# Performance work log

Hardware: AMD Instinct MI355X
Metric: run time of the kernel (lower is better)

The kernel has to match this reference:

```python
import jax, jax.numpy as jnp
import numpy as np

N_QUBITS = 11
N_CIRCUITS = 3
N_ROTS = 6
BATCH = 512
C64 = jnp.complex64


def _ry_mat(theta):
    # RY(t) = [[cos t/2, -sin t/2], [sin t/2, cos t/2]]
    c = jnp.cos(theta * 0.5)
    s = jnp.sin(theta * 0.5)
    return jnp.stack([jnp.stack([c, -s]), jnp.stack([s, c])]).astype(C64)


def _rz_mat(theta):
    # RZ(t) = diag(e^{-i t/2}, e^{+i t/2})
    e = jnp.exp((-0.5j) * theta.astype(C64))
    z = jnp.zeros_like(e)
    return jnp.stack([jnp.stack([e, z]), jnp.stack([z, jnp.conj(e)])])


def _apply_1q(state, U, q):
    # state: (2,)*n complex; apply 2x2 U on axis q (PennyLane wire q = axis q)
    out = jnp.tensordot(U, state, axes=((1,), (q,)))
    return jnp.moveaxis(out, 0, q)


def _apply_ctrl(state, U, c, t):
    # controlled-U on wires [c(control), t(target)]: block_diag(I2, U) in |c t> basis
    U4 = jnp.eye(4, dtype=C64).at[2:, 2:].set(U)
    out = jnp.tensordot(U4.reshape(2, 2, 2, 2), state, axes=((2, 3), (c, t)))
    return jnp.moveaxis(out, (0, 1), (c, t))


def _simulate(angles):
    # angles: [n_circuits, 6, n_qubits] -> expvals [2*n_qubits] (X then Z)
    n = N_QUBITS
    state = jnp.zeros((2,) * n, dtype=C64).at[(0,) * n].set(1.0)
    for i in range(N_CIRCUITS):
        for q in range(n):
            state = _apply_1q(state, _ry_mat(angles[i, 0, q]), q)
            state = _apply_1q(state, _rz_mat(angles[i, 1, q]), q)
            state = _apply_1q(state, _ry_mat(angles[i, 2, q]), q)
            state = _apply_1q(state, _rz_mat(angles[i, 3, q]), q)
        for q in range(n):
            t = (q + 1) % n
            state = _apply_ctrl(state, _ry_mat(angles[i, 4, q]), q, t)
            state = _apply_ctrl(state, _rz_mat(angles[i, 5, q]), q, t)
    ex_x, ex_z = [], []
    for q in range(n):
        s0 = jnp.take(state, 0, axis=q)
        s1 = jnp.take(state, 1, axis=q)
        # <X_q> = 2 Re <psi_{q=0}|psi_{q=1}>,  <Z_q> = p(q=0) - p(q=1)
        ex_x.append(2.0 * jnp.real(jnp.vdot(s0, s1)))
        ex_z.append(jnp.sum(jnp.abs(s0) ** 2 - jnp.abs(s1) ** 2))
    return jnp.stack(ex_x + ex_z).astype(jnp.float32)


def setup_inputs() -> dict:
    key = jax.random.key(0)
    k1, k2, k3 = jax.random.split(key, 3)
    x = jax.random.normal(k1, (BATCH, N_QUBITS), dtype=jnp.float32)
    W = jax.random.uniform(k2, (N_CIRCUITS, N_QUBITS * N_ROTS, N_QUBITS),
                           dtype=jnp.float32, minval=-0.01, maxval=0.01)
    b = jax.random.uniform(k3, (N_CIRCUITS, N_QUBITS * N_ROTS),
                           dtype=jnp.float32, minval=-0.01, maxval=0.01)
    return {"x": x, "W": W, "b": b}


def reference(x, W, b):
    # per-circuit Linear (dropout is identity in eval): [B, C, n_rots*n_qubits]
    rot = jnp.einsum('coi,bi->bco', W, x) + b[None, :, :]
    angles = rot.reshape(x.shape[0], N_CIRCUITS, N_ROTS, N_QUBITS)
    return jax.vmap(_simulate)(angles)  # [B, 2*n_qubits]
```

## Files before the change

### kernel.cpp

```cpp
#include <hip/hip_runtime.h>

#define NQ 11
#define NC 3
#define NANG (NC * 66)
#define BLOCK 1024

typedef float f2 __attribute__((ext_vector_type(2)));

__device__ __forceinline__ f2 swp(f2 v) { return __builtin_shufflevector(v, v, 1, 0); }

template<int CTRL>
__device__ __forceinline__ float dppx(float v) {
  return __int_as_float(__builtin_amdgcn_update_dpp(
      0, __float_as_int(v), CTRL, 0xF, 0xF, false));
}
template<int CTRL>
__device__ __forceinline__ f2 dpp2(f2 v) {
  f2 r; r.x = dppx<CTRL>(v.x); r.y = dppx<CTRL>(v.y); return r;
}
template<int OFF>
__device__ __forceinline__ float swz1(float v) {
  return __int_as_float(__builtin_amdgcn_ds_swizzle(__float_as_int(v), OFF));
}
template<int OFF>
__device__ __forceinline__ f2 swz2(f2 v) {
  f2 r; r.x = swz1<OFF>(v.x); r.y = swz1<OFF>(v.y); return r;
}
__device__ __forceinline__ float plp16(float v, int lane) {
  auto r = __builtin_amdgcn_permlane16_swap(__float_as_int(v), __float_as_int(v), false, false);
  return __int_as_float((lane & 16) ? r[0] : r[1]);
}
__device__ __forceinline__ float plp32(float v, int lane) {
  auto r = __builtin_amdgcn_permlane32_swap(__float_as_int(v), __float_as_int(v), false, false);
  return __int_as_float((lane & 32) ? r[0] : r[1]);
}
__device__ __forceinline__ f2 plp16_2(f2 v, int lane) {
  f2 r; r.x = plp16(v.x, lane); r.y = plp16(v.y, lane); return r;
}
__device__ __forceinline__ f2 plp32_2(f2 v, int lane) {
  f2 r; r.x = plp32(v.x, lane); r.y = plp32(v.y, lane); return r;
}
__device__ __forceinline__ float plsum16(float v) {
  auto r = __builtin_amdgcn_permlane16_swap(__float_as_int(v), __float_as_int(v), false, false);
  return __int_as_float(r[0]) + __int_as_float(r[1]);
}
__device__ __forceinline__ float plsum32(float v) {
  auto r = __builtin_amdgcn_permlane32_swap(__float_as_int(v), __float_as_int(v), false, false);
  return __int_as_float(r[0]) + __int_as_float(r[1]);
}

__device__ __forceinline__ void apply2p(f2& v0, f2& v1, float4 U) {
  const f2 ai2 = {-U.y, U.y};
  const f2 bi2 = {-U.w, U.w};
  const f2 w0 = swp(v0), w1 = swp(v1);
  const f2 n0 =  U.x * v0 + ai2 * w0 + U.z * v1 + bi2 * w1;
  const f2 n1 = -U.z * v0 + bi2 * w0 + U.x * v1 - ai2 * w1;
  v0 = n0; v1 = n1;
}
__device__ __forceinline__ void gpartp(f2& v, f2 p, float4 U, bool hi) {
  const f2 ai2 = hi ? f2{U.y, -U.y} : f2{-U.y, U.y};
  const float br = hi ? -U.z : U.z;
  const f2 bi2 = {-U.w, U.w};
  v = U.x * v + ai2 * swp(v) + br * p + bi2 * swp(p);
}

template<int WVX>
__device__ __forceinline__ void g_wave(f2& s0, f2& s1, float4 U,
                                       f2* __restrict__ buf, int wave, int lane) {
  const int idx = (wave << 6) | lane;
  buf[idx] = s0; buf[1024 + idx] = s1;
  __syncthreads();
  const int p = ((wave ^ WVX) << 6) | lane;
  const bool hi = (wave & WVX) != 0;
  gpartp(s0, buf[p], U, hi);
  gpartp(s1, buf[1024 + p], U, hi);
}

__global__ __launch_bounds__(BLOCK, 8) void qsim_kernel(
    const float* __restrict__ x, const float* __restrict__ W,
    const float* __restrict__ bias, float* __restrict__ out) {
  const int bidx = blockIdx.x;
  const int tid = threadIdx.x;
  const int lane = tid & 63, wave = tid >> 6;

  __shared__ float xs[NQ];
  __shared__ float ang[NANG];
  __shared__ float4 m1s[NC * NQ];
  __shared__ float4 m2s[NC * NQ];
  __shared__ float4 v1s[NC * 10];
  __shared__ f2 ex0[2048];
  __shared__ f2 ex1[2048];
  __shared__ float red[16][24];

  if (tid < NQ) xs[tid] = x[bidx * NQ + tid];
  __syncthreads();

  if (tid < NANG) {
    const int c = tid / 66, o = tid - c * 66;
    const float* wr = W + (c * 66 + o) * NQ;
    float s = bias[c * 66 + o];
#pragma unroll
    for (int i = 0; i < NQ; ++i) s += wr[i] * xs[i];
    ang[tid] = s;
  }
  __syncthreads();

  if (tid < 2 * NC * NQ) {
    const int kind = tid / (NC * NQ);
    const int id = tid - kind * (NC * NQ);
    const int c = id / NQ, q = id - c * NQ;
    const float* a = ang + c * 66;
    if (kind == 0) {
      float s0,c0,s1,c1,s2,c2,s3,c3;
      sincosf(0.5f*a[q],      &s0,&c0);
      sincosf(0.5f*a[11+q],   &s1,&c1);
      sincosf(0.5f*a[22+q],   &s2,&c2);
      sincosf(0.5f*a[33+q],   &s3,&c3);
      const float mar = c1*c0, mai = -s1*c0;
      const float mbr = -c1*s0, mbi = s1*s0;
      const float nar = c2*mar + s2*mbr, nai = c2*mai - s2*mbi;
      const float nbr = c2*mbr - s2*mar, nbi = c2*mbi + s2*mai;
      m1s[id] = make_float4(c3*nar + s3*nai, c3*nai - s3*nar,
                            c3*nbr + s3*nbi, c3*nbi - s3*nbr);
    } else {
      float s4,c4,s5,c5;
      sincosf(0.5f*a[44+q], &s4,&c4);
      sincosf(0.5f*a[55+q], &s5,&c5);
      m2s[id] = make_float4(c5*c4, -s5*c4, -c5*s4, s5*s4);
    }
  }
  __syncthreads();

  if (tid < NC * 10) {
    const int c = tid / 10, tt = tid - c * 10, t = tt + 1;
    const float4 A = m2s[c*NQ + t - 1];
    const float4 B = m1s[c*NQ + t];
    const float pr_=A.x, pi_=A.y, qr_=A.z, qi_=A.w;
    const float ar_=B.x, ai_=B.y, br_=B.z, bi_=B.w;
    v1s[c*10 + tt] = make_float4(
      (pr_*ar_ - pi_*ai_) - (qr_*br_ + qi_*bi_),
      (pr_*ai_ + pi_*ar_) - (qi_*br_ - qr_*bi_),
      (pr_*br_ - pi_*bi_) + (qr_*ar_ + qi_*ai_),
      (pr_*bi_ + pi_*br_) + (qi_*ar_ - qr_*ai_));
  }
  __syncthreads();

  f2 s0 = {0.f, 0.f}, s1 = {0.f, 0.f};
  if (tid == 0) s0.x = 1.f;

  for (int c = 0; c < NC; ++c) {
    const float4* M1 = &m1s[c * NQ];
    const float4* VF = &v1s[c * 10];
    apply2p(s0, s1, M1[0]);
    {
      const bool hi = (lane & 32) != 0;
      gpartp(s0, plp32_2(s0, lane), M1[1], hi);
      gpartp(s1, plp32_2(s1, lane), VF[0], hi);
    }
    {
      const float4 U = *((lane & 32) ? &VF[1] : &M1[2]);
      const bool hi = (lane & 16) != 0;
      gpartp(s0, plp16_2(s0, lane), U, hi);
      gpartp(s1, plp16_2(s1, lane), U, hi);
    }
    {
      const float4 U = *((lane & 16) ? &VF[2] : &M1[3]);
      const bool hi = (lane & 8) != 0;
      gpartp(s0, swz2<0x201F>(s0), U, hi);
      gpartp(s1, swz2<0x201F>(s1), U, hi);
    }
    g_wave<8>(s0, s1, *((lane & 8) ? &VF[3] : &M1[4]), ex0, wave, lane);
    g_wave<4>(s0, s1, *((wave & 8) ? &VF[4] : &M1[5]), ex1, wave, lane);
    g_wave<2>(s0, s1, *((wave & 4) ? &VF[5] : &M1[6]), ex0, wave, lane);
    g_wave<1>(s0, s1, *((wave & 2) ? &VF[6] : &M1[7]), ex1, wave, lane);
    {
      const float4 U = *((wave & 1) ? &VF[7] : &M1[8]);
      const bool hi = (lane & 4) != 0;
      gpartp(s0, swz2<0x101F>(s0), U, hi);
      gpartp(s1, swz2<0x101F>(s1), U, hi);
    }
    {
      const float4 U = *((lane & 4) ? &VF[8] : &M1[9]);
      const bool hi = (lane & 2) != 0;
      gpartp(s0, dpp2<0x4E>(s0), U, hi);
      gpartp(s1, dpp2<0x4E>(s1), U, hi);
    }
    {
      const float4 U = *((lane & 2) ? &VF[9] : &M1[10]);
      const bool hi = (lane & 1) != 0;
      gpartp(s0, dpp2<0xB1>(s0), U, hi);
      gpartp(s1, dpp2<0xB1>(s1), U, hi);
    }
    {
      const float4 Uc = m2s[c * NQ + 10];
      const float4 U = (lane & 1) ? Uc : make_float4(1.f, 0.f, 0.f, 0.f);
      apply2p(s0, s1, U);
    }
  }

  const int idx = (wave << 6) | lane;
  ex0[idx] = s0; ex0[1024 + idx] = s1;
  __syncthreads();
  const int p8 = ((wave ^ 8) << 6) | lane;
  const int p4 = ((wave ^ 4) << 6) | lane;
  const int p2 = ((wave ^ 2) << 6) | lane;
  const int p1 = ((wave ^ 1) << 6) | lane;
  f2 t;
  t = s0*ex0[p8] + s1*ex0[1024+p8]; const float xq4 = t.x + t.y;
  t = s0*ex0[p4] + s1*ex0[1024+p4]; const float xq5 = t.x + t.y;
  t = s0*ex0[p2] + s1*ex0[1024+p2]; const float xq6 = t.x + t.y;
  t = s0*ex0[p1] + s1*ex0[1024+p1]; const float xq7 = t.x + t.y;

  const f2 mg0 = s0 * s0, mg1 = s1 * s1;
  const float m0 = mg0.x + mg0.y, m1 = mg1.x + mg1.y;
  const float ztot = m0 + m1;
  const float zq0 = m0 - m1;
  t = s0 * s1; const float xq0 = 2.f * (t.x + t.y);
  t = s0*plp32_2(s0,lane) + s1*plp32_2(s1,lane); const float xq1 = t.x + t.y;
  t = s0*plp16_2(s0,lane) + s1*plp16_2(s1,lane); const float xq2 = t.x + t.y;
  t = s0*swz2<0x201F>(s0) + s1*swz2<0x201F>(s1); const float xq3 = t.x + t.y;
  t = s0*swz2<0x101F>(s0) + s1*swz2<0x101F>(s1); const float xq8 = t.x + t.y;
  t = s0*dpp2<0x4E>(s0)  + s1*dpp2<0x4E>(s1);  const float xq9 = t.x + t.y;
  t = s0*dpp2<0xB1>(s0)  + s1*dpp2<0xB1>(s1);  const float xq10 = t.x + t.y;

  float v[22];
  v[0]=xq0; v[1]=xq1; v[2]=xq2; v[3]=xq3; v[4]=xq4; v[5]=xq5; v[6]=xq6;
  v[7]=xq7; v[8]=xq8; v[9]=xq9; v[10]=xq10;
  v[11] = zq0;
  v[12] = (lane & 32) ? -ztot : ztot;
  v[13] = (lane & 16) ? -ztot : ztot;
  v[14] = (lane & 8)  ? -ztot : ztot;
  v[15] = (wave & 8)  ? -ztot : ztot;
  v[16] = (wave & 4)  ? -ztot : ztot;
  v[17] = (wave & 2)  ? -ztot : ztot;
  v[18] = (wave & 1)  ? -ztot : ztot;
  v[19] = (lane & 4)  ? -ztot : ztot;
  v[20] = (lane & 2)  ? -ztot : ztot;
  v[21] = (lane & 1)  ? -ztot : ztot;

#pragma unroll
  for (int k = 0; k < 22; ++k) {
    v[k] += dppx<0xB1>(v[k]);
    v[k] += dppx<0x4E>(v[k]);
  }
  const int q4l = lane & 3;
  float wv[6];
#pragma unroll
  for (int p = 0; p < 5; ++p)
    wv[p] = q4l == 0 ? v[4*p] : (q4l == 1 ? v[4*p+1] : (q4l == 2 ? v[4*p+2] : v[4*p+3]));
  wv[5] = q4l == 0 ? v[20] : (q4l == 1 ? v[21] : 0.f);
#pragma unroll
  for (int p = 0; p < 6; ++p) {
    wv[p] += swz1<0x101F>(wv[p]);
    wv[p] += swz1<0x201F>(wv[p]);
    wv[p] = plsum16(wv[p]);
    wv[p] = plsum32(wv[p]);
  }
  if (lane < 4) {
#pragma unroll
    for (int p = 0; p < 6; ++p) red[wave][4*p + lane] = wv[p];
  }
  __syncthreads();
  if (tid < 22) {
    float sacc = 0.f;
#pragma unroll
    for (int w16 = 0; w16 < 16; ++w16) sacc += red[w16][tid];
    out[bidx * 22 + tid] = sacc;
  }
}

extern "C" void kernel_launch(void* const* d_in, const int* in_sizes, int n_in,
                              void* d_out, int out_size, void* d_ws, size_t ws_size,
                              hipStream_t stream) {
  (void)n_in; (void)d_ws; (void)ws_size; (void)out_size;
  const float* x = (const float*)d_in[0];
  const float* W = (const float*)d_in[1];
  const float* b = (const float*)d_in[2];
  float* out = (float*)d_out;
  const int batch = in_sizes[0] / NQ;
  qsim_kernel<<<batch, BLOCK, 0, stream>>>(x, W, b, out);
}
```

Baseline: 24.27 us.

## Hold full statevector in one wavefront with 32 amplitudes per lane

Shrinks each block from 1024 threads to a single 64-lane wavefront. Each lane now keeps 32 complex amplitudes in registers, and the qubit mapping is changed so that 6 qubits are handled by cross-lane DPP, swizzle and permute ops while 5 are handled in-register. This removes all LDS exchange buffers, the __syncthreads between gate stages and the cross-wave final reduction. The cost is much higher register pressure, which may cause spills or low occupancy, and only 512 single-wave blocks are launched, so fewer threads hide latency.

```diff
diff --git a/kernel.cpp b/kernel.cpp
--- a/kernel.cpp
+++ b/kernel.cpp
@@ -3,7 +3,7 @@
 #define NQ 11
 #define NC 3
 #define NANG (NC * 66)
-#define BLOCK 1024
+#define BLOCK 64
 
 typedef float f2 __attribute__((ext_vector_type(2)));
 
@@ -64,53 +64,43 @@
   v = U.x * v + ai2 * swp(v) + br * p + bi2 * swp(p);
 }
 
-template<int WVX>
-__device__ __forceinline__ void g_wave(f2& s0, f2& s1, float4 U,
-                                       f2* __restrict__ buf, int wave, int lane) {
-  const int idx = (wave << 6) | lane;
-  buf[idx] = s0; buf[1024 + idx] = s1;
-  __syncthreads();
-  const int p = ((wave ^ WVX) << 6) | lane;
-  const bool hi = (wave & WVX) != 0;
-  gpartp(s0, buf[p], U, hi);
-  gpartp(s1, buf[1024 + p], U, hi);
-}
-
-__global__ __launch_bounds__(BLOCK, 8) void qsim_kernel(
+__global__ __launch_bounds__(BLOCK) void qsim_kernel(
     const float* __restrict__ x, const float* __restrict__ W,
     const float* __restrict__ bias, float* __restrict__ out) {
   const int bidx = blockIdx.x;
-  const int tid = threadIdx.x;
-  const int lane = tid & 63, wave = tid >> 6;
+  const int lane = threadIdx.x;
 
   __shared__ float xs[NQ];
   __shared__ float ang[NANG];
   __shared__ float4 m1s[NC * NQ];
   __shared__ float4 m2s[NC * NQ];
   __shared__ float4 v1s[NC * 10];
-  __shared__ f2 ex0[2048];
-  __shared__ f2 ex1[2048];
-  __shared__ float red[16][24];
-
-  if (tid < NQ) xs[tid] = x[bidx * NQ + tid];
+
+  if (lane < NQ) xs[lane] = x[bidx * NQ + lane];
   __syncthreads();
 
-  if (tid < NANG) {
-    const int c = tid / 66, o = tid - c * 66;
-    const float* wr = W + (c * 66 + o) * NQ;
-    float s = bias[c * 66 + o];
-#pragma unroll
-    for (int i = 0; i < NQ; ++i) s += wr[i] * xs[i];
-    ang[tid] = s;
+#pragma unroll
+  for (int r4 = 0; r4 < 4; ++r4) {
+    const int id = lane + 64 * r4;
+    if (id < NANG) {
+      const int c = id / 66, o = id - c * 66;
+      const float* wr = W + (c * 66 + o) * NQ;
+      float s = bias[c * 66 + o];
+#pragma unroll
+      for (int i = 0; i < NQ; ++i) s += wr[i] * xs[i];
+      ang[id] = s;
+    }
   }
   __syncthreads();
 
-  if (tid < 2 * NC * NQ) {
-    const int kind = tid / (NC * NQ);
-    const int id = tid - kind * (NC * NQ);
-    const int c = id / NQ, q = id - c * NQ;
-    const float* a = ang + c * 66;
-    if (kind == 0) {
+#pragma unroll
+  for (int pass = 0; pass < 2; ++pass) {
+    int id; bool do1 = false, do2 = false;
+    if (pass == 0) { if (lane < 33) { do1 = true; id = lane; } else { do2 = true; id = lane - 33; } }
+    else { if (lane < 2) { do2 = true; id = 31 + lane; } }
+    if (do1) {
+      const int c = id / NQ, q = id - c * NQ;
+      const float* a = ang + c * 66;
       float s0,c0,s1,c1,s2,c2,s3,c3;
       sincosf(0.5f*a[q],      &s0,&c0);
       sincosf(0.5f*a[11+q],   &s1,&c1);
@@ -122,7 +112,10 @@
       const float nbr = c2*mbr - s2*mar, nbi = c2*mbi + s2*mai;
       m1s[id] = make_float4(c3*nar + s3*nai, c3*nai - s3*nar,
                             c3*nbr + s3*nbi, c3*nbi - s3*nbr);
-    } else {
+    }
+    if (do2) {
+      const int c = id / NQ, q = id - c * NQ;
+      const float* a = ang + c * 66;
       float s4,c4,s5,c5;
       sincosf(0.5f*a[44+q], &s4,&c4);
       sincosf(0.5f*a[55+q], &s5,&c5);
@@ -131,8 +124,8 @@
   }
   __syncthreads();
 
-  if (tid < NC * 10) {
-    const int c = tid / 10, tt = tid - c * 10, t = tt + 1;
+  if (lane < NC * 10) {
+    const int c = lane / 10, tt = lane - c * 10, t = tt + 1;
     const float4 A = m2s[c*NQ + t - 1];
     const float4 B = m1s[c*NQ + t];
     const float pr_=A.x, pi_=A.y, qr_=A.z, qi_=A.w;
@@ -145,98 +138,140 @@
   }
   __syncthreads();
 
-  f2 s0 = {0.f, 0.f}, s1 = {0.f, 0.f};
-  if (tid == 0) s0.x = 1.f;
+  f2 s[32];
+#pragma unroll
+  for (int r = 0; r < 32; ++r) s[r] = f2{0.f, 0.f};
+  if (lane == 0) s[0].x = 1.f;
 
   for (int c = 0; c < NC; ++c) {
     const float4* M1 = &m1s[c * NQ];
     const float4* VF = &v1s[c * 10];
-    apply2p(s0, s1, M1[0]);
-    {
+    {
+      const float4 U = M1[0];
       const bool hi = (lane & 32) != 0;
-      gpartp(s0, plp32_2(s0, lane), M1[1], hi);
-      gpartp(s1, plp32_2(s1, lane), VF[0], hi);
-    }
-    {
-      const float4 U = *((lane & 32) ? &VF[1] : &M1[2]);
+#pragma unroll
+      for (int r = 0; r < 32; ++r) gpartp(s[r], plp32_2(s[r], lane), U, hi);
+    }
+    {
+      const float4 U = *((lane & 32) ? &VF[0] : &M1[1]);
       const bool hi = (lane & 16) != 0;
-      gpartp(s0, plp16_2(s0, lane), U, hi);
-      gpartp(s1, plp16_2(s1, lane), U, hi);
-    }
-    {
-      const float4 U = *((lane & 16) ? &VF[2] : &M1[3]);
+#pragma unroll
+      for (int r = 0; r < 32; ++r) gpartp(s[r], plp16_2(s[r], lane), U, hi);
+    }
+    {
+      const float4 U = *((lane & 16) ? &VF[1] : &M1[2]);
       const bool hi = (lane & 8) != 0;
-      gpartp(s0, swz2<0x201F>(s0), U, hi);
-      gpartp(s1, swz2<0x201F>(s1), U, hi);
-    }
-    g_wave<8>(s0, s1, *((lane & 8) ? &VF[3] : &M1[4]), ex0, wave, lane);
-    g_wave<4>(s0, s1, *((wave & 8) ? &VF[4] : &M1[5]), ex1, wave, lane);
-    g_wave<2>(s0, s1, *((wave & 4) ? &VF[5] : &M1[6]), ex0, wave, lane);
-    g_wave<1>(s0, s1, *((wave & 2) ? &VF[6] : &M1[7]), ex1, wave, lane);
-    {
-      const float4 U = *((wave & 1) ? &VF[7] : &M1[8]);
+#pragma unroll
+      for (int r = 0; r < 32; ++r) gpartp(s[r], swz2<0x201F>(s[r]), U, hi);
+    }
+    {
+      const float4 U = *((lane & 8) ? &VF[2] : &M1[3]);
       const bool hi = (lane & 4) != 0;
-      gpartp(s0, swz2<0x101F>(s0), U, hi);
-      gpartp(s1, swz2<0x101F>(s1), U, hi);
-    }
-    {
-      const float4 U = *((lane & 4) ? &VF[8] : &M1[9]);
+#pragma unroll
+      for (int r = 0; r < 32; ++r) gpartp(s[r], swz2<0x101F>(s[r]), U, hi);
+    }
+    {
+      const float4 U = *((lane & 4) ? &VF[3] : &M1[4]);
       const bool hi = (lane & 2) != 0;
-      gpartp(s0, dpp2<0x4E>(s0), U, hi);
-      gpartp(s1, dpp2<0x4E>(s1), U, hi);
-    }
-    {
-      const float4 U = *((lane & 2) ? &VF[9] : &M1[10]);
+#pragma unroll
+      for (int r = 0; r < 32; ++r) gpartp(s[r], dpp2<0x4E>(s[r]), U, hi);
+    }
+    {
+      const float4 U = *((lane & 2) ? &VF[4] : &M1[5]);
       const bool hi = (lane & 1) != 0;
-      gpartp(s0, dpp2<0xB1>(s0), U, hi);
-      gpartp(s1, dpp2<0xB1>(s1), U, hi);
-    }
-    {
-      const float4 Uc = m2s[c * NQ + 10];
-      const float4 U = (lane & 1) ? Uc : make_float4(1.f, 0.f, 0.f, 0.f);
-      apply2p(s0, s1, U);
-    }
-  }
-
-  const int idx = (wave << 6) | lane;
-  ex0[idx] = s0; ex0[1024 + idx] = s1;
-  __syncthreads();
-  const int p8 = ((wave ^ 8) << 6) | lane;
-  const int p4 = ((wave ^ 4) << 6) | lane;
-  const int p2 = ((wave ^ 2) << 6) | lane;
-  const int p1 = ((wave ^ 1) << 6) | lane;
-  f2 t;
-  t = s0*ex0[p8] + s1*ex0[1024+p8]; const float xq4 = t.x + t.y;
-  t = s0*ex0[p4] + s1*ex0[1024+p4]; const float xq5 = t.x + t.y;
-  t = s0*ex0[p2] + s1*ex0[1024+p2]; const float xq6 = t.x + t.y;
-  t = s0*ex0[p1] + s1*ex0[1024+p1]; const float xq7 = t.x + t.y;
-
-  const f2 mg0 = s0 * s0, mg1 = s1 * s1;
-  const float m0 = mg0.x + mg0.y, m1 = mg1.x + mg1.y;
-  const float ztot = m0 + m1;
-  const float zq0 = m0 - m1;
-  t = s0 * s1; const float xq0 = 2.f * (t.x + t.y);
-  t = s0*plp32_2(s0,lane) + s1*plp32_2(s1,lane); const float xq1 = t.x + t.y;
-  t = s0*plp16_2(s0,lane) + s1*plp16_2(s1,lane); const float xq2 = t.x + t.y;
-  t = s0*swz2<0x201F>(s0) + s1*swz2<0x201F>(s1); const float xq3 = t.x + t.y;
-  t = s0*swz2<0x101F>(s0) + s1*swz2<0x101F>(s1); const float xq8 = t.x + t.y;
-  t = s0*dpp2<0x4E>(s0)  + s1*dpp2<0x4E>(s1);  const float xq9 = t.x + t.y;
-  t = s0*dpp2<0xB1>(s0)  + s1*dpp2<0xB1>(s1);  const float xq10 = t.x + t.y;
+#pragma unroll
+      for (int r = 0; r < 32; ++r) gpartp(s[r], dpp2<0xB1>(s[r]), U, hi);
+    }
+    {
+      const float4 U = *((lane & 1) ? &VF[5] : &M1[6]);
+#pragma unroll
+      for (int r = 0; r < 16; ++r) apply2p(s[r], s[r | 16], U);
+    }
+    {
+      const float4 U0 = M1[7], U1 = VF[6];
+#pragma unroll
+      for (int r = 0; r < 32; ++r) {
+        if (r & 8) continue;
+        apply2p(s[r], s[r | 8], (r & 16) ? U1 : U0);
+      }
+    }
+    {
+      const float4 U0 = M1[8], U1 = VF[7];
+#pragma unroll
+      for (int r = 0; r < 32; ++r) {
+        if (r & 4) continue;
+        apply2p(s[r], s[r | 4], (r & 8) ? U1 : U0);
+      }
+    }
+    {
+      const float4 U0 = M1[9], U1 = VF[8];
+#pragma unroll
+      for (int r = 0; r < 32; ++r) {
+        if (r & 2) continue;
+        apply2p(s[r], s[r | 2], (r & 4) ? U1 : U0);
+      }
+    }
+    {
+      const float4 U0 = M1[10], U1 = VF[9];
+#pragma unroll
+      for (int r = 0; r < 32; ++r) {
+        if (r & 1) continue;
+        apply2p(s[r], s[r | 1], (r & 2) ? U1 : U0);
+      }
+    }
+    {
+      const float4 U = m2s[c * NQ + 10];
+      const bool hi = (lane & 32) != 0;
+#pragma unroll
+      for (int r = 1; r < 32; r += 2) gpartp(s[r], plp32_2(s[r], lane), U, hi);
+    }
+  }
+
+  f2 zt = {0,0}, z6 = {0,0}, z7 = {0,0}, z8 = {0,0}, z9 = {0,0}, z10 = {0,0};
+#pragma unroll
+  for (int r = 0; r < 32; ++r) {
+    const f2 m = s[r] * s[r];
+    zt += m;
+    z6  += (r & 16) ? -m : m;
+    z7  += (r & 8)  ? -m : m;
+    z8  += (r & 4)  ? -m : m;
+    z9  += (r & 2)  ? -m : m;
+    z10 += (r & 1)  ? -m : m;
+  }
+  f2 x6 = {0,0}, x7 = {0,0}, x8 = {0,0}, x9 = {0,0}, x10 = {0,0};
+#pragma unroll
+  for (int r = 0; r < 32; ++r) {
+    x6  += s[r] * s[r ^ 16];
+    x7  += s[r] * s[r ^ 8];
+    x8  += s[r] * s[r ^ 4];
+    x9  += s[r] * s[r ^ 2];
+    x10 += s[r] * s[r ^ 1];
+  }
+  f2 x0 = {0,0}, x1 = {0,0}, x2 = {0,0}, x3 = {0,0}, x4 = {0,0}, x5 = {0,0};
+#pragma unroll
+  for (int r = 0; r < 32; ++r) {
+    x0 += s[r] * plp32_2(s[r], lane);
+    x1 += s[r] * plp16_2(s[r], lane);
+    x2 += s[r] * swz2<0x201F>(s[r]);
+    x3 += s[r] * swz2<0x101F>(s[r]);
+    x4 += s[r] * dpp2<0x4E>(s[r]);
+    x5 += s[r] * dpp2<0xB1>(s[r]);
+  }
+  const float zts = zt.x + zt.y;
 
   float v[22];
-  v[0]=xq0; v[1]=xq1; v[2]=xq2; v[3]=xq3; v[4]=xq4; v[5]=xq5; v[6]=xq6;
-  v[7]=xq7; v[8]=xq8; v[9]=xq9; v[10]=xq10;
-  v[11] = zq0;
-  v[12] = (lane & 32) ? -ztot : ztot;
-  v[13] = (lane & 16) ? -ztot : ztot;
-  v[14] = (lane & 8)  ? -ztot : ztot;
-  v[15] = (wave & 8)  ? -ztot : ztot;
-  v[16] = (wave & 4)  ? -ztot : ztot;
-  v[17] = (wave & 2)  ? -ztot : ztot;
-  v[18] = (wave & 1)  ? -ztot : ztot;
-  v[19] = (lane & 4)  ? -ztot : ztot;
-  v[20] = (lane & 2)  ? -ztot : ztot;
-  v[21] = (lane & 1)  ? -ztot : ztot;
+  v[0] = x0.x + x0.y;  v[1] = x1.x + x1.y;  v[2] = x2.x + x2.y;
+  v[3] = x3.x + x3.y;  v[4] = x4.x + x4.y;  v[5] = x5.x + x5.y;
+  v[6] = x6.x + x6.y;  v[7] = x7.x + x7.y;  v[8] = x8.x + x8.y;
+  v[9] = x9.x + x9.y;  v[10] = x10.x + x10.y;
+  v[11] = (lane & 32) ? -zts : zts;
+  v[12] = (lane & 16) ? -zts : zts;
+  v[13] = (lane & 8)  ? -zts : zts;
+  v[14] = (lane & 4)  ? -zts : zts;
+  v[15] = (lane & 2)  ? -zts : zts;
+  v[16] = (lane & 1)  ? -zts : zts;
+  v[17] = z6.x + z6.y;  v[18] = z7.x + z7.y;  v[19] = z8.x + z8.y;
+  v[20] = z9.x + z9.y;  v[21] = z10.x + z10.y;
 
 #pragma unroll
   for (int k = 0; k < 22; ++k) {
@@ -258,14 +293,8 @@
   }
   if (lane < 4) {
 #pragma unroll
-    for (int p = 0; p < 6; ++p) red[wave][4*p + lane] = wv[p];
-  }
-  __syncthreads();
-  if (tid < 22) {
-    float sacc = 0.f;
-#pragma unroll
-    for (int w16 = 0; w16 < 16; ++w16) sacc += red[w16][tid];
-    out[bidx * 22 + tid] = sacc;
+    for (int p = 0; p < 5; ++p) out[bidx * 22 + 4*p + lane] = wv[p];
+    if (lane < 2) out[bidx * 22 + 20 + lane] = wv[5];
   }
 }
 
```

After: 33.77 us. 39.1% more time.
